# Kernel tuning notes

Measured on AMD Instinct MI355X. Metric: run time of the kernel, lower is better.

The kernel has to match this reference:

```python
import jax, jax.numpy as jnp
import numpy as np

B, N, IN_DIM = 64, 4096, 128
D = 128          # slot_size
S = 7            # num_slots
ITERS = 3
HID = 256        # mlp_hdim
EPS = 1e-8       # renorm epsilon
LN_EPS = 1e-5    # torch LayerNorm default


def _ln(x, g, b):
    m = jnp.mean(x, axis=-1, keepdims=True)
    v = jnp.mean((x - m) ** 2, axis=-1, keepdims=True)
    return (x - m) * jax.lax.rsqrt(v + LN_EPS) * g + b


def setup_inputs() -> dict:
    key = jax.random.key(0)
    ks = jax.random.split(key, 16)
    s = 0.02
    return {
        "x": jax.random.normal(ks[0], (B, N, IN_DIM), jnp.float32),
        "noise": jax.random.normal(ks[1], (B, S, D), jnp.float32),
        "Wq": jax.random.normal(ks[2], (D, D), jnp.float32) * s,
        "Wk": jax.random.normal(ks[3], (D, IN_DIM), jnp.float32) * s,
        "Wv": jax.random.normal(ks[4], (D, IN_DIM), jnp.float32) * s,
        "ln_in_g": jnp.ones((IN_DIM,), jnp.float32),
        "ln_in_b": jnp.zeros((IN_DIM,), jnp.float32),
        "ln_slots_g": jnp.ones((D,), jnp.float32),
        "ln_slots_b": jnp.zeros((D,), jnp.float32),
        "ln_mlp_g": jnp.ones((D,), jnp.float32),
        "ln_mlp_b": jnp.zeros((D,), jnp.float32),
        "W_ih": jax.random.normal(ks[5], (3 * D, D), jnp.float32) * s,
        "W_hh": jax.random.normal(ks[6], (3 * D, D), jnp.float32) * s,
        "b_ih": jnp.zeros((3 * D,), jnp.float32),
        "b_hh": jnp.zeros((3 * D,), jnp.float32),
        "W1": jax.random.normal(ks[7], (HID, D), jnp.float32) * s,
        "b1": jnp.zeros((HID,), jnp.float32),
        "W2": jax.random.normal(ks[8], (D, HID), jnp.float32) * s,
        "b2": jnp.zeros((D,), jnp.float32),
        "mu": jax.random.normal(ks[9], (1, 1, D), jnp.float32) * s,
        "logsigma": jax.random.normal(ks[10], (1, D), jnp.float32) * s,
    }


def reference(x, noise, Wq, Wk, Wv, ln_in_g, ln_in_b, ln_slots_g, ln_slots_b,
              ln_mlp_g, ln_mlp_b, W_ih, W_hh, b_ih, b_hh, W1, b1, W2, b2,
              mu, logsigma):
    xn = _ln(x, ln_in_g, ln_in_b)              # (B,N,IN)
    k = xn @ Wk.T                              # (B,N,D)
    v = xn @ Wv.T                              # (B,N,D)

    scale = jax.nn.softplus(logsigma)[None] + 1e-5   # (1,1,D)
    slots = mu + scale * noise                 # rsample, (B,S,D)

    def gru(u, h):
        gx = u @ W_ih.T + b_ih                 # (B*S, 3D)
        gh = h @ W_hh.T + b_hh
        xr, xz, xn_ = jnp.split(gx, 3, axis=-1)
        hr, hz, hn = jnp.split(gh, 3, axis=-1)
        r = jax.nn.sigmoid(xr + hr)
        z = jax.nn.sigmoid(xz + hz)
        n = jnp.tanh(xn_ + r * hn)
        return (1.0 - z) * n + z * h

    inv_sqrt_d = D ** -0.5
    for _ in range(ITERS):
        slots_prev = slots
        sn = _ln(slots, ln_slots_g, ln_slots_b)
        q = sn @ Wq.T                          # (B,S,D)
        scores = inv_sqrt_d * jnp.einsum('bnd,bsd->bns', k, q)
        attn = jax.nn.softmax(scores, axis=-1)           # over slots
        attn = attn + EPS
        attn = attn / jnp.sum(attn, axis=1, keepdims=True)  # renorm over inputs
        updates = jnp.einsum('bns,bnd->bsd', attn, v)    # (B,S,D)
        h = gru(updates.reshape(-1, D), slots_prev.reshape(-1, D))
        slots = h.reshape(x.shape[0], S, D)
        slots = _ln(slots, ln_mlp_g, ln_mlp_b)
        slots = slots + (jax.nn.relu(slots @ W1.T + b1) @ W2.T + b2)
    return slots
```

## Files before the change

### kernel.cpp

```cpp
#include <hip/hip_runtime.h>
#include <hip/hip_bf16.h>
#include <stdint.h>

#define B_ 64
#define N_ 4096
#define D_ 128
#define S_ 7
#define EPS_ 1e-8f
#define LN_EPS_ 1e-5f

typedef float  f32x4  __attribute__((ext_vector_type(4)));
typedef __bf16 bf16x8 __attribute__((ext_vector_type(8)));

#define WIH_OFF 0
#define WHH_OFF 49152
#define W1_OFF  98304
#define W2_OFF  131072
#define WQ_OFF  163840
#define WBF_TOT 180224

__device__ __forceinline__ uint16_t f2bfbits(float f) {
    uint32_t x = __float_as_uint(f);
    return (uint16_t)((x + 0x7fffu + ((x >> 16) & 1u)) >> 16);
}
__device__ __forceinline__ uint32_t pk2(float a, float b) {
    return (uint32_t)f2bfbits(a) | ((uint32_t)f2bfbits(b) << 16);
}

__global__ __launch_bounds__(256) void k_prep(
    const float* __restrict__ noise, const float* __restrict__ Wk,
    const float* __restrict__ Wv, const float* __restrict__ mu,
    const float* __restrict__ logsigma, const float* __restrict__ Wq,
    const float* __restrict__ lsg, const float* __restrict__ lsb,
    const float* __restrict__ Wih, const float* __restrict__ Whh,
    const float* __restrict__ W1, const float* __restrict__ W2,
    uint16_t* __restrict__ Wsw, float* __restrict__ slots,
    uint16_t* __restrict__ qbf, uint16_t* __restrict__ wbf) {
    const int t = threadIdx.x;
    const int tid = blockIdx.x * 256 + t;
    __shared__ float sn[128];
    __shared__ float red[2];
    {
        int row = blockIdx.x;
        int b = row / 7, s = row - b * 7;
        bool act = t < 128;
        float v = 0.f;
        if (act) {
            float sc = log1pf(__expf(logsigma[t])) + 1e-5f;
            v = mu[t] + sc * noise[row * 128 + t];
            slots[row * 128 + t] = v;
        }
        float sv = act ? v : 0.f;
        #pragma unroll
        for (int m = 1; m < 64; m <<= 1) sv += __shfl_xor(sv, m);
        if (act && (t & 63) == 0) red[t >> 6] = sv;
        __syncthreads();
        float mean = (red[0] + red[1]) * (1.0f / 128.0f);
        __syncthreads();
        float dv = act ? (v - mean) : 0.f;
        float sq = dv * dv;
        #pragma unroll
        for (int m = 1; m < 64; m <<= 1) sq += __shfl_xor(sq, m);
        if (act && (t & 63) == 0) red[t >> 6] = sq;
        __syncthreads();
        float var = (red[0] + red[1]) * (1.0f / 128.0f);
        if (act) sn[t] = dv * rsqrtf(var + LN_EPS_) * lsg[t] + lsb[t];
        __syncthreads();
        if (act) {
            const float4* wr = (const float4*)(Wq + t * 128);
            float acc = 0.f;
            #pragma unroll 8
            for (int j = 0; j < 32; ++j) {
                float4 w = wr[j];
                float4 s4 = *(const float4*)(sn + 4 * j);
                acc += w.x * s4.x + w.y * s4.y + w.z * s4.z + w.w * s4.w;
            }
            qbf[(b * 16 + s) * 128 + t] = f2bfbits(acc * 0.08838834764831843f);
        }
    }
    if (tid < 32768) {
        int j = tid & 7, ch = tid >> 3;
        int lane = ch & 63, k0 = (ch >> 6) & 3, wt = (ch >> 8) & 7, h = ch >> 11;
        int row = wt * 16 + (lane & 15);
        int col = k0 * 32 + (lane >> 4) * 8 + j;
        float w = h ? Wv[row * 128 + col] : Wk[row * 128 + col];
        Wsw[tid] = f2bfbits(w);
    }
    if (tid < 73728) {
        int bb = tid / 1152, rem = tid - bb * 1152;
        int s = 7 + (rem >> 7), d = rem & 127;
        qbf[(bb * 16 + s) * 128 + d] = 0;
    }
    for (int e = tid; e < WBF_TOT; e += 448 * 256) {
        const float* W; int C, el;
        if (e < WHH_OFF)      { W = Wih; C = 128; el = e; }
        else if (e < W1_OFF)  { W = Whh; C = 128; el = e - WHH_OFF; }
        else if (e < W2_OFF)  { W = W1;  C = 128; el = e - W1_OFF; }
        else if (e < WQ_OFF)  { W = W2;  C = 256; el = e - W2_OFF; }
        else                  { W = Wq;  C = 128; el = e - WQ_OFF; }
        int tile = el >> 9, within = el & 511;
        int lp = within >> 3, j = within & 7;
        int lm = lp & 15, qd = lp >> 4;
        int ktN = C >> 5;
        int ot = tile / ktN, kt = tile - ot * ktN;
        wbf[e] = f2bfbits(W[(ot * 16 + lm) * C + kt * 32 + qd * 8 + j]);
    }
}

__global__ __launch_bounds__(256) void k_proj(
    const float* __restrict__ x, const uint16_t* __restrict__ Wsw,
    const float* __restrict__ lng, const float* __restrict__ lnb,
    uint16_t* __restrict__ kfrag, uint16_t* __restrict__ vfrag) {
    __shared__ __align__(16) uint16_t wlds[16384];
    const int t = threadIdx.x, wv = t >> 6, lane = t & 63;
    const int lm = lane & 15, qd = lane >> 4;
    const long row0 = (long)blockIdx.x * 64;
    const int b = (int)(row0 >> 12);
    const int nloc = (int)(row0 & 4095);

    uint4 wst[8];
    #pragma unroll
    for (int i = 0; i < 8; ++i)
        wst[i] = *(const uint4*)(Wsw + (i * 256 + t) * 8);

    const long xrow = row0 + wv * 16 + lm;
    const float* xp = x + xrow * 128 + qd * 8;
    f32x4 xa[8];
    #pragma unroll
    for (int k0 = 0; k0 < 4; ++k0) {
        xa[2 * k0]     = *(const f32x4*)(xp + k0 * 32);
        xa[2 * k0 + 1] = *(const f32x4*)(xp + k0 * 32 + 4);
    }
    #pragma unroll
    for (int i = 0; i < 8; ++i)
        *(uint4*)(wlds + (i * 256 + t) * 8) = wst[i];
    #pragma unroll
    for (int i = 0; i < 8; ++i)
        wst[i] = *(const uint4*)(Wsw + 16384 + (i * 256 + t) * 8);

    float s = 0.f, sq = 0.f;
    #pragma unroll
    for (int i = 0; i < 8; ++i)
        #pragma unroll
        for (int c = 0; c < 4; ++c) { float v = xa[i][c]; s += v; sq += v * v; }
    s  += __shfl_xor(s, 16);  s  += __shfl_xor(s, 32);
    sq += __shfl_xor(sq, 16); sq += __shfl_xor(sq, 32);
    float mean = s * (1.0f / 128.0f);
    float var  = sq * (1.0f / 128.0f) - mean * mean;
    float rs   = rsqrtf(var + LN_EPS_);

    bf16x8 xf[4];
    #pragma unroll
    for (int k0 = 0; k0 < 4; ++k0) {
        const float* gp = lng + k0 * 32 + qd * 8;
        const float* bp = lnb + k0 * 32 + qd * 8;
        f32x4 g0 = *(const f32x4*)(gp), g1 = *(const f32x4*)(gp + 4);
        f32x4 b0 = *(const f32x4*)(bp), b1 = *(const f32x4*)(bp + 4);
        #pragma unroll
        for (int c = 0; c < 4; ++c) {
            xf[k0][c]     = (__bf16)((xa[2 * k0][c]     - mean) * rs * g0[c] + b0[c]);
            xf[k0][4 + c] = (__bf16)((xa[2 * k0 + 1][c] - mean) * rs * g1[c] + b1[c]);
        }
    }
    __syncthreads();

    const int ntg = (int)(row0 >> 4) + wv;
    #pragma unroll
    for (int mt = 0; mt < 8; ++mt) {
        f32x4 acc = {0.f, 0.f, 0.f, 0.f};
        #pragma unroll
        for (int k0 = 0; k0 < 4; ++k0) {
            bf16x8 wf = *(const bf16x8*)(wlds + ((mt * 4 + k0) * 64 + lane) * 8);
            acc = __builtin_amdgcn_mfma_f32_16x16x32_bf16(wf, xf[k0], acc, 0, 0, 0);
        }
        uint2 st; st.x = pk2(acc[0], acc[1]); st.y = pk2(acc[2], acc[3]);
        long base = ((long)(ntg * 4 + (mt >> 1))) * 512
                  + (lm + 16 * ((2 * mt + (qd >> 1)) & 3)) * 8 + (qd & 1) * 4;
        *(uint2*)(kfrag + base) = st;
    }
    __syncthreads();

    #pragma unroll
    for (int i = 0; i < 8; ++i)
        *(uint4*)(wlds + (i * 256 + t) * 8) = wst[i];
    __syncthreads();

    #pragma unroll
    for (int nt = 0; nt < 8; ++nt) {
        f32x4 acc = {0.f, 0.f, 0.f, 0.f};
        #pragma unroll
        for (int k0 = 0; k0 < 4; ++k0) {
            bf16x8 wf = *(const bf16x8*)(wlds + ((nt * 4 + k0) * 64 + lane) * 8);
            acc = __builtin_amdgcn_mfma_f32_16x16x32_bf16(xf[k0], wf, acc, 0, 0, 0);
        }
        uint2 st; st.x = pk2(acc[0], acc[1]); st.y = pk2(acc[2], acc[3]);
        long tile = (long)(b * 8 + nt) * 128 + (nloc >> 5) + (wv >> 1);
        long base = tile * 512
                  + (lm + 16 * (((wv & 1) * 2 + (qd >> 1)) & 3)) * 8 + (qd & 1) * 4;
        *(uint2*)(vfrag + base) = st;
    }
}

__global__ __launch_bounds__(512) void k_attn(
    const uint16_t* __restrict__ kfrag, const uint16_t* __restrict__ vfrag,
    const uint16_t* __restrict__ qbf,
    float* __restrict__ upart, float* __restrict__ cpart) {
    __shared__ __align__(16) uint16_t als[8][1024];
    __shared__ __align__(16) float part[8][7][132];
    __shared__ float bsum[8][8];
    const int t = threadIdx.x, wv = t >> 6, lane = t & 63;
    const int lm = lane & 15, qd = lane >> 4;
    const int b = blockIdx.x >> 3, chunk = blockIdx.x & 7;
    const int rb = chunk * 512 + wv * 64;
    const long gn = (long)b * N_ + rb;

    bf16x8 bq[4];
    #pragma unroll
    for (int k0 = 0; k0 < 4; ++k0)
        bq[k0] = *(const bf16x8*)(qbf + b * 2048 + lm * 128 + k0 * 32 + qd * 8);

    float csl = 0.f;
    #pragma unroll
    for (int mt = 0; mt < 4; ++mt) {
        f32x4 acc = {0.f, 0.f, 0.f, 0.f};
        long tb = ((gn >> 4) + mt) * 4;
        #pragma unroll
        for (int k0 = 0; k0 < 4; ++k0) {
            bf16x8 a = *(const bf16x8*)(kfrag + (tb + k0) * 512 + lane * 8);
            acc = __builtin_amdgcn_mfma_f32_16x16x32_bf16(a, bq[k0], acc, 0, 0, 0);
        }
        uint16_t pb[4];
        #pragma unroll
        for (int r = 0; r < 4; ++r) {
            float sc = acc[r];
            float scm = (lm < 7) ? sc : -1e30f;
            #pragma unroll
            for (int m = 1; m < 16; m <<= 1) scm = fmaxf(scm, __shfl_xor(scm, m));
            float e = (lm < 7) ? __expf(sc - scm) : 0.f;
            float tot = e;
            #pragma unroll
            for (int m = 1; m < 16; m <<= 1) tot += __shfl_xor(tot, m);
            float a_ = e / tot + EPS_;
            if (lm < 7) csl += a_;
            pb[r] = f2bfbits(a_);
        }
        int elem = (mt >> 1) * 512 + (((mt & 1) * 2 + (qd >> 1)) * 16 + lm) * 8 + (qd & 1) * 4;
        uint2 pw; pw.x = (uint32_t)pb[0] | ((uint32_t)pb[1] << 16);
        pw.y = (uint32_t)pb[2] | ((uint32_t)pb[3] << 16);
        *(uint2*)(&als[wv][elem]) = pw;
    }
    csl += __shfl_xor(csl, 16); csl += __shfl_xor(csl, 32);
    if (lane < 7) bsum[wv][lane] = csl;
    __syncthreads();

    bf16x8 afr0 = *(const bf16x8*)(&als[wv][lane * 8]);
    bf16x8 afr1 = *(const bf16x8*)(&als[wv][512 + lane * 8]);
    f32x4 uacc[8];
    #pragma unroll
    for (int i = 0; i < 8; ++i) uacc[i] = (f32x4){0.f, 0.f, 0.f, 0.f};
    #pragma unroll
    for (int nt = 0; nt < 8; ++nt) {
        long tb = ((long)(b * 8 + nt) * 128 + (rb >> 5)) * 512;
        bf16x8 v0 = *(const bf16x8*)(vfrag + tb + lane * 8);
        bf16x8 v1 = *(const bf16x8*)(vfrag + tb + 512 + lane * 8);
        uacc[nt] = __builtin_amdgcn_mfma_f32_16x16x32_bf16(v0, afr0, uacc[nt], 0, 0, 0);
        uacc[nt] = __builtin_amdgcn_mfma_f32_16x16x32_bf16(v1, afr1, uacc[nt], 0, 0, 0);
    }
    if (lm < 7) {
        #pragma unroll
        for (int nt = 0; nt < 8; ++nt)
            *(f32x4*)&part[wv][lm][nt * 16 + qd * 4] = uacc[nt];
    }
    __syncthreads();
    if (t < 128) {
        #pragma unroll
        for (int s = 0; s < 7; ++s) {
            float v = 0.f;
            #pragma unroll
            for (int w = 0; w < 8; ++w) v += part[w][s][t];
            upart[((b * 8 + chunk) * 7 + s) * 128 + t] = v;
        }
    }
    if (t < 7) {
        float c = 0.f;
        #pragma unroll
        for (int w = 0; w < 8; ++w) c += bsum[w][t];
        cpart[(b * 8 + chunk) * 7 + t] = c;
    }
}

__global__ __launch_bounds__(256) void k_fused(
    const float* __restrict__ upart, const float* __restrict__ cpart,
    float* __restrict__ slots, const uint16_t* __restrict__ wbf,
    const float* __restrict__ bih, const float* __restrict__ bhh,
    const float* __restrict__ gm, const float* __restrict__ bm,
    const float* __restrict__ b1, const float* __restrict__ b2,
    const float* __restrict__ lsg, const float* __restrict__ lsb,
    uint16_t* __restrict__ qbf, float* __restrict__ dst, int hasq) {
    __shared__ float uf[16][132];
    __shared__ float hf[16][132];
    __shared__ float slf[16][132];
    __shared__ float hidl[16][264];
    __shared__ float glg[7][776];
    __shared__ float csl[7];
    const int b = blockIdx.x;
    const int t = threadIdx.x, wv = t >> 6, lane = t & 63;
    const int lm = lane & 15, qd = lane >> 4;

    if (t < 7) {
        float c = 0.f;
        #pragma unroll
        for (int i = 0; i < 8; ++i) c += cpart[(b * 8 + i) * 7 + t];
        csl[t] = c;
    }
    __syncthreads();
    for (int idx = t; idx < 896; idx += 256) {
        int s = idx >> 7, d = idx & 127;
        float acc = 0.f;
        #pragma unroll
        for (int i = 0; i < 8; ++i) acc += upart[((b * 8 + i) * 7 + s) * 128 + d];
        uf[s][d] = acc / csl[s];
        hf[s][d] = slots[(b * 7 + s) * 128 + d];
    }
    __syncthreads();

    bf16x8 au[4], ah[4];
    #pragma unroll
    for (int k0 = 0; k0 < 4; ++k0)
        #pragma unroll
        for (int j = 0; j < 8; ++j) {
            au[k0][j] = (__bf16)uf[lm][k0 * 32 + qd * 8 + j];
            ah[k0][j] = (__bf16)hf[lm][k0 * 32 + qd * 8 + j];
        }

    {
        const int ih = (wv < 2);
        const uint16_t* W = wbf + (ih ? WIH_OFF : WHH_OFF);
        const int base = ih ? 0 : 384;
        const int w2 = wv & 1;
        #pragma unroll
        for (int i = 0; i < 12; ++i) {
            int ot = w2 * 12 + i;
            f32x4 acc = {0.f, 0.f, 0.f, 0.f};
            #pragma unroll
            for (int k0 = 0; k0 < 4; ++k0) {
                bf16x8 bf = *(const bf16x8*)(W + ((ot * 4 + k0) << 9) + lane * 8);
                acc = __builtin_amdgcn_mfma_f32_16x16x32_bf16(ih ? au[k0] : ah[k0], bf, acc, 0, 0, 0);
            }
            #pragma unroll
            for (int r = 0; r < 4; ++r) {
                int s = qd * 4 + r;
                if (s < 7) glg[s][base + ot * 16 + lm] = acc[r];
            }
        }
    }
    __syncthreads();

    for (int idx = t; idx < 896; idx += 256) {
        int s = idx >> 7, d = idx & 127;
        float xr = glg[s][d] + bih[d];
        float xz = glg[s][128 + d] + bih[128 + d];
        float xn = glg[s][256 + d] + bih[256 + d];
        float hr = glg[s][384 + d] + bhh[d];
        float hz = glg[s][512 + d] + bhh[128 + d];
        float hnn = glg[s][640 + d] + bhh[256 + d];
        float r = 1.f / (1.f + __expf(-(xr + hr)));
        float z = 1.f / (1.f + __expf(-(xz + hz)));
        float n = tanhf(xn + r * hnn);
        uf[s][d] = (1.f - z) * n + z * hf[s][d];
    }
    __syncthreads();

    for (int s = wv; s < 7; s += 4) {
        float a0 = uf[s][2 * lane], a1 = uf[s][2 * lane + 1];
        float sm = a0 + a1, sq = a0 * a0 + a1 * a1;
        #pragma unroll
        for (int m = 1; m < 64; m <<= 1) { sm += __shfl_xor(sm, m); sq += __shfl_xor(sq, m); }
        float mean = sm * (1.0f / 128.0f);
        float var = sq * (1.0f / 128.0f) - mean * mean;
        float rs = rsqrtf(var + LN_EPS_);
        slf[s][2 * lane]     = (a0 - mean) * rs * gm[2 * lane] + bm[2 * lane];
        slf[s][2 * lane + 1] = (a1 - mean) * rs * gm[2 * lane + 1] + bm[2 * lane + 1];
    }
    __syncthreads();

    bf16x8 as_[4];
    #pragma unroll
    for (int k0 = 0; k0 < 4; ++k0)
        #pragma unroll
        for (int j = 0; j < 8; ++j) as_[k0][j] = (__bf16)slf[lm][k0 * 32 + qd * 8 + j];
    #pragma unroll
    for (int i = 0; i < 4; ++i) {
        int ot = wv * 4 + i;
        f32x4 acc = {0.f, 0.f, 0.f, 0.f};
        #pragma unroll
        for (int k0 = 0; k0 < 4; ++k0) {
            bf16x8 bf = *(const bf16x8*)(wbf + W1_OFF + ((ot * 4 + k0) << 9) + lane * 8);
            acc = __builtin_amdgcn_mfma_f32_16x16x32_bf16(as_[k0], bf, acc, 0, 0, 0);
        }
        #pragma unroll
        for (int r = 0; r < 4; ++r) {
            int s = qd * 4 + r;
            if (s < 7) hidl[s][ot * 16 + lm] = fmaxf(acc[r] + b1[ot * 16 + lm], 0.f);
        }
    }
    __syncthreads();

    bf16x8 ahd[8];
    #pragma unroll
    for (int k0 = 0; k0 < 8; ++k0)
        #pragma unroll
        for (int j = 0; j < 8; ++j) ahd[k0][j] = (__bf16)hidl[lm][k0 * 32 + qd * 8 + j];
    #pragma unroll
    for (int i = 0; i < 2; ++i) {
        int ot = wv * 2 + i;
        f32x4 acc = {0.f, 0.f, 0.f, 0.f};
        #pragma unroll
        for (int k0 = 0; k0 < 8; ++k0) {
            bf16x8 bf = *(const bf16x8*)(wbf + W2_OFF + ((ot * 8 + k0) << 9) + lane * 8);
            acc = __builtin_amdgcn_mfma_f32_16x16x32_bf16(ahd[k0], bf, acc, 0, 0, 0);
        }
        #pragma unroll
        for (int r = 0; r < 4; ++r) {
            int s = qd * 4 + r;
            if (s < 7) {
                float v = slf[s][ot * 16 + lm] + acc[r] + b2[ot * 16 + lm];
                hf[s][ot * 16 + lm] = v;
                dst[(b * 7 + s) * 128 + ot * 16 + lm] = v;
            }
        }
    }
    if (hasq) {
        __syncthreads();
        for (int s = wv; s < 7; s += 4) {
            float a0 = hf[s][2 * lane], a1 = hf[s][2 * lane + 1];
            float sm = a0 + a1, sq = a0 * a0 + a1 * a1;
            #pragma unroll
            for (int m = 1; m < 64; m <<= 1) { sm += __shfl_xor(sm, m); sq += __shfl_xor(sq, m); }
            float mean = sm * (1.0f / 128.0f);
            float var = sq * (1.0f / 128.0f) - mean * mean;
            float rs = rsqrtf(var + LN_EPS_);
            uf[s][2 * lane]     = (a0 - mean) * rs * lsg[2 * lane] + lsb[2 * lane];
            uf[s][2 * lane + 1] = (a1 - mean) * rs * lsg[2 * lane + 1] + lsb[2 * lane + 1];
        }
        __syncthreads();
        bf16x8 an[4];
        #pragma unroll
        for (int k0 = 0; k0 < 4; ++k0)
            #pragma unroll
            for (int j = 0; j < 8; ++j) an[k0][j] = (__bf16)uf[lm][k0 * 32 + qd * 8 + j];
        #pragma unroll
        for (int i = 0; i < 2; ++i) {
            int ot = wv * 2 + i;
            f32x4 acc = {0.f, 0.f, 0.f, 0.f};
            #pragma unroll
            for (int k0 = 0; k0 < 4; ++k0) {
                bf16x8 bf = *(const bf16x8*)(wbf + WQ_OFF + ((ot * 4 + k0) << 9) + lane * 8);
                acc = __builtin_amdgcn_mfma_f32_16x16x32_bf16(an[k0], bf, acc, 0, 0, 0);
            }
            #pragma unroll
            for (int r = 0; r < 4; ++r) {
                int s = qd * 4 + r;
                if (s < 7)
                    qbf[(b * 16 + s) * 128 + ot * 16 + lm] = f2bfbits(acc[r] * 0.08838834764831843f);
            }
        }
    }
}

extern "C" void kernel_launch(void* const* d_in, const int* in_sizes, int n_in,
                              void* d_out, int out_size, void* d_ws, size_t ws_size,
                              hipStream_t stream) {
    const float* x    = (const float*)d_in[0];
    const float* nz   = (const float*)d_in[1];
    const float* Wq   = (const float*)d_in[2];
    const float* Wk   = (const float*)d_in[3];
    const float* Wv   = (const float*)d_in[4];
    const float* ling = (const float*)d_in[5];
    const float* linb = (const float*)d_in[6];
    const float* lsg  = (const float*)d_in[7];
    const float* lsb  = (const float*)d_in[8];
    const float* lmg  = (const float*)d_in[9];
    const float* lmb  = (const float*)d_in[10];
    const float* Wih  = (const float*)d_in[11];
    const float* Whh  = (const float*)d_in[12];
    const float* bih  = (const float*)d_in[13];
    const float* bhh  = (const float*)d_in[14];
    const float* W1   = (const float*)d_in[15];
    const float* b1   = (const float*)d_in[16];
    const float* W2   = (const float*)d_in[17];
    const float* b2   = (const float*)d_in[18];
    const float* mu   = (const float*)d_in[19];
    const float* lsig = (const float*)d_in[20];

    char* wsb = (char*)d_ws;
    uint16_t* kfrag = (uint16_t*)(wsb);
    uint16_t* vfrag = (uint16_t*)(wsb + (size_t)67108864);
    uint16_t* Wsw   = (uint16_t*)(wsb + (size_t)134217728);
    uint16_t* qbf   = (uint16_t*)(wsb + (size_t)134283264);
    float*    slots = (float*)  (wsb + (size_t)134545408);
    float*    upart = (float*)  (wsb + (size_t)134774784);
    float*    cpart = (float*)  (wsb + (size_t)136609792);
    uint16_t* wbf   = (uint16_t*)(wsb + (size_t)136624128);

    k_prep<<<448, 256, 0, stream>>>(nz, Wk, Wv, mu, lsig, Wq, lsg, lsb,
                                    Wih, Whh, W1, W2, Wsw, slots, qbf, wbf);
    k_proj<<<4096, 256, 0, stream>>>(x, Wsw, ling, linb, kfrag, vfrag);
    for (int it = 0; it < 3; ++it) {
        float* dst = (it == 2) ? (float*)d_out : slots;
        k_attn<<<512, 512, 0, stream>>>(kfrag, vfrag, qbf, upart, cpart);
        k_fused<<<64, 256, 0, stream>>>(upart, cpart, slots, wbf, bih, bhh,
                                        lmg, lmb, b1, b2, lsg, lsb,
                                        qbf, dst, (it < 2) ? 1 : 0);
    }
}
```

Baseline: 414.3 us.

## Fold Wk into query and Wv into update; attend directly over normalized inputs

```diff
diff --git a/kernel.cpp b/kernel.cpp
--- a/kernel.cpp
+++ b/kernel.cpp
@@ -8,6 +8,7 @@
 #define S_ 7
 #define EPS_ 1e-8f
 #define LN_EPS_ 1e-5f
+#define SC_INV 0.08838834764831843f
 
 typedef float  f32x4  __attribute__((ext_vector_type(4)));
 typedef __bf16 bf16x8 __attribute__((ext_vector_type(8)));
@@ -17,7 +18,9 @@
 #define W1_OFF  98304
 #define W2_OFF  131072
 #define WQ_OFF  163840
-#define WBF_TOT 180224
+#define WKT_OFF 180224
+#define WV_OFF  196608
+#define WBF_TOT 212992
 
 __device__ __forceinline__ uint16_t f2bfbits(float f) {
     uint32_t x = __float_as_uint(f);
@@ -27,266 +30,226 @@
     return (uint32_t)f2bfbits(a) | ((uint32_t)f2bfbits(b) << 16);
 }
 
-__global__ __launch_bounds__(256) void k_prep(
+__global__ __launch_bounds__(256) void k_init(
     const float* __restrict__ noise, const float* __restrict__ Wk,
-    const float* __restrict__ Wv, const float* __restrict__ mu,
-    const float* __restrict__ logsigma, const float* __restrict__ Wq,
-    const float* __restrict__ lsg, const float* __restrict__ lsb,
+    const float* __restrict__ mu, const float* __restrict__ logsigma,
+    const float* __restrict__ Wq, const float* __restrict__ lsg,
+    const float* __restrict__ lsb,
     const float* __restrict__ Wih, const float* __restrict__ Whh,
     const float* __restrict__ W1, const float* __restrict__ W2,
-    uint16_t* __restrict__ Wsw, float* __restrict__ slots,
-    uint16_t* __restrict__ qbf, uint16_t* __restrict__ wbf) {
+    const float* __restrict__ Wv,
+    float* __restrict__ slots, uint16_t* __restrict__ kqbf,
+    uint16_t* __restrict__ wbf) {
     const int t = threadIdx.x;
     const int tid = blockIdx.x * 256 + t;
-    __shared__ float sn[128];
+    const int row = blockIdx.x;
+    const int b = row / 7, s = row - b * 7;
+    __shared__ float sn[128], qr[128];
     __shared__ float red[2];
-    {
-        int row = blockIdx.x;
-        int b = row / 7, s = row - b * 7;
-        bool act = t < 128;
-        float v = 0.f;
-        if (act) {
-            float sc = log1pf(__expf(logsigma[t])) + 1e-5f;
-            v = mu[t] + sc * noise[row * 128 + t];
-            slots[row * 128 + t] = v;
-        }
-        float sv = act ? v : 0.f;
-        #pragma unroll
-        for (int m = 1; m < 64; m <<= 1) sv += __shfl_xor(sv, m);
-        if (act && (t & 63) == 0) red[t >> 6] = sv;
-        __syncthreads();
-        float mean = (red[0] + red[1]) * (1.0f / 128.0f);
-        __syncthreads();
-        float dv = act ? (v - mean) : 0.f;
-        float sq = dv * dv;
-        #pragma unroll
-        for (int m = 1; m < 64; m <<= 1) sq += __shfl_xor(sq, m);
-        if (act && (t & 63) == 0) red[t >> 6] = sq;
-        __syncthreads();
-        float var = (red[0] + red[1]) * (1.0f / 128.0f);
-        if (act) sn[t] = dv * rsqrtf(var + LN_EPS_) * lsg[t] + lsb[t];
-        __syncthreads();
-        if (act) {
-            const float4* wr = (const float4*)(Wq + t * 128);
-            float acc = 0.f;
-            #pragma unroll 8
-            for (int j = 0; j < 32; ++j) {
-                float4 w = wr[j];
-                float4 s4 = *(const float4*)(sn + 4 * j);
-                acc += w.x * s4.x + w.y * s4.y + w.z * s4.z + w.w * s4.w;
-            }
-            qbf[(b * 16 + s) * 128 + t] = f2bfbits(acc * 0.08838834764831843f);
-        }
-    }
-    if (tid < 32768) {
-        int j = tid & 7, ch = tid >> 3;
-        int lane = ch & 63, k0 = (ch >> 6) & 3, wt = (ch >> 8) & 7, h = ch >> 11;
-        int row = wt * 16 + (lane & 15);
-        int col = k0 * 32 + (lane >> 4) * 8 + j;
-        float w = h ? Wv[row * 128 + col] : Wk[row * 128 + col];
-        Wsw[tid] = f2bfbits(w);
+    bool act = t < 128;
+    float v = 0.f;
+    if (act) {
+        float sc = log1pf(__expf(logsigma[t])) + 1e-5f;
+        v = mu[t] + sc * noise[row * 128 + t];
+        slots[row * 128 + t] = v;
+    }
+    float sv = act ? v : 0.f;
+    #pragma unroll
+    for (int m = 1; m < 64; m <<= 1) sv += __shfl_xor(sv, m);
+    if (act && (t & 63) == 0) red[t >> 6] = sv;
+    __syncthreads();
+    float mean = (red[0] + red[1]) * (1.0f / 128.0f);
+    __syncthreads();
+    float dv = act ? (v - mean) : 0.f;
+    float sq = dv * dv;
+    #pragma unroll
+    for (int m = 1; m < 64; m <<= 1) sq += __shfl_xor(sq, m);
+    if (act && (t & 63) == 0) red[t >> 6] = sq;
+    __syncthreads();
+    float var = (red[0] + red[1]) * (1.0f / 128.0f);
+    if (act) sn[t] = dv * rsqrtf(var + LN_EPS_) * lsg[t] + lsb[t];
+    __syncthreads();
+    if (act) {
+        const float4* wr = (const float4*)(Wq + t * 128);
+        float acc = 0.f;
+        #pragma unroll 8
+        for (int j = 0; j < 32; ++j) {
+            float4 w = wr[j];
+            float4 s4 = *(const float4*)(sn + 4 * j);
+            acc += w.x * s4.x + w.y * s4.y + w.z * s4.z + w.w * s4.w;
+        }
+        qr[t] = acc;
+    }
+    __syncthreads();
+    if (act) {
+        float kq = 0.f;
+        #pragma unroll 8
+        for (int o = 0; o < 128; ++o) kq += qr[o] * Wk[o * 128 + t];
+        int elem = (t >> 5) * 512 + (s + 16 * ((t >> 3) & 3)) * 8 + (t & 7);
+        kqbf[b * 2048 + elem] = f2bfbits(kq * SC_INV);
     }
     if (tid < 73728) {
         int bb = tid / 1152, rem = tid - bb * 1152;
-        int s = 7 + (rem >> 7), d = rem & 127;
-        qbf[(bb * 16 + s) * 128 + d] = 0;
+        int sp = 7 + (rem >> 7), d = rem & 127;
+        int elem = (d >> 5) * 512 + (sp + 16 * ((d >> 3) & 3)) * 8 + (d & 7);
+        kqbf[bb * 2048 + elem] = 0;
     }
     for (int e = tid; e < WBF_TOT; e += 448 * 256) {
-        const float* W; int C, el;
+        const float* W; int C, el, mode = 0;
         if (e < WHH_OFF)      { W = Wih; C = 128; el = e; }
         else if (e < W1_OFF)  { W = Whh; C = 128; el = e - WHH_OFF; }
         else if (e < W2_OFF)  { W = W1;  C = 128; el = e - W1_OFF; }
         else if (e < WQ_OFF)  { W = W2;  C = 256; el = e - W2_OFF; }
-        else                  { W = Wq;  C = 128; el = e - WQ_OFF; }
+        else if (e < WKT_OFF) { W = Wq;  C = 128; el = e - WQ_OFF; }
+        else if (e < WV_OFF)  { W = Wk;  C = 128; el = e - WKT_OFF; mode = 1; }
+        else                  { W = Wv;  C = 128; el = e - WV_OFF; }
         int tile = el >> 9, within = el & 511;
         int lp = within >> 3, j = within & 7;
-        int lm = lp & 15, qd = lp >> 4;
-        int ktN = C >> 5;
-        int ot = tile / ktN, kt = tile - ot * ktN;
-        wbf[e] = f2bfbits(W[(ot * 16 + lm) * C + kt * 32 + qd * 8 + j]);
-    }
-}
-
-__global__ __launch_bounds__(256) void k_proj(
-    const float* __restrict__ x, const uint16_t* __restrict__ Wsw,
-    const float* __restrict__ lng, const float* __restrict__ lnb,
-    uint16_t* __restrict__ kfrag, uint16_t* __restrict__ vfrag) {
-    __shared__ __align__(16) uint16_t wlds[16384];
+        int lm_ = lp & 15, qd_ = lp >> 4;
+        float w;
+        if (!mode) {
+            int ktN = C >> 5, ot = tile / ktN, kt = tile - ot * ktN;
+            w = W[(ot * 16 + lm_) * C + kt * 32 + qd_ * 8 + j];
+        } else {
+            int dt = tile >> 2, kt = tile & 3;
+            w = W[(kt * 32 + qd_ * 8 + j) * 128 + dt * 16 + lm_];
+        }
+        wbf[e] = f2bfbits(w);
+    }
+}
+
+__global__ __launch_bounds__(256) void k_prep_xn(
+    const float* __restrict__ x, const float* __restrict__ lng,
+    const float* __restrict__ lnb, uint16_t* __restrict__ xn) {
     const int t = threadIdx.x, wv = t >> 6, lane = t & 63;
     const int lm = lane & 15, qd = lane >> 4;
-    const long row0 = (long)blockIdx.x * 64;
-    const int b = (int)(row0 >> 12);
-    const int nloc = (int)(row0 & 4095);
-
-    uint4 wst[8];
-    #pragma unroll
-    for (int i = 0; i < 8; ++i)
-        wst[i] = *(const uint4*)(Wsw + (i * 256 + t) * 8);
-
-    const long xrow = row0 + wv * 16 + lm;
-    const float* xp = x + xrow * 128 + qd * 8;
+    const long row = (long)blockIdx.x * 64 + wv * 16 + lm;
+    const long ntile = (long)blockIdx.x * 4 + wv;
+    const float* xp = x + row * 128 + qd * 4;
     f32x4 xa[8];
     #pragma unroll
-    for (int k0 = 0; k0 < 4; ++k0) {
-        xa[2 * k0]     = *(const f32x4*)(xp + k0 * 32);
-        xa[2 * k0 + 1] = *(const f32x4*)(xp + k0 * 32 + 4);
-    }
-    #pragma unroll
-    for (int i = 0; i < 8; ++i)
-        *(uint4*)(wlds + (i * 256 + t) * 8) = wst[i];
-    #pragma unroll
-    for (int i = 0; i < 8; ++i)
-        wst[i] = *(const uint4*)(Wsw + 16384 + (i * 256 + t) * 8);
-
+    for (int c = 0; c < 8; ++c) xa[c] = *(const f32x4*)(xp + c * 16);
     float s = 0.f, sq = 0.f;
     #pragma unroll
-    for (int i = 0; i < 8; ++i)
-        #pragma unroll
-        for (int c = 0; c < 4; ++c) { float v = xa[i][c]; s += v; sq += v * v; }
+    for (int c = 0; c < 8; ++c)
+        #pragma unroll
+        for (int r = 0; r < 4; ++r) { float v = xa[c][r]; s += v; sq += v * v; }
     s  += __shfl_xor(s, 16);  s  += __shfl_xor(s, 32);
     sq += __shfl_xor(sq, 16); sq += __shfl_xor(sq, 32);
     float mean = s * (1.0f / 128.0f);
     float var  = sq * (1.0f / 128.0f) - mean * mean;
     float rs   = rsqrtf(var + LN_EPS_);
-
-    bf16x8 xf[4];
-    #pragma unroll
-    for (int k0 = 0; k0 < 4; ++k0) {
-        const float* gp = lng + k0 * 32 + qd * 8;
-        const float* bp = lnb + k0 * 32 + qd * 8;
-        f32x4 g0 = *(const f32x4*)(gp), g1 = *(const f32x4*)(gp + 4);
-        f32x4 b0 = *(const f32x4*)(bp), b1 = *(const f32x4*)(bp + 4);
-        #pragma unroll
-        for (int c = 0; c < 4; ++c) {
-            xf[k0][c]     = (__bf16)((xa[2 * k0][c]     - mean) * rs * g0[c] + b0[c]);
-            xf[k0][4 + c] = (__bf16)((xa[2 * k0 + 1][c] - mean) * rs * g1[c] + b1[c]);
-        }
-    }
-    __syncthreads();
-
-    const int ntg = (int)(row0 >> 4) + wv;
-    #pragma unroll
-    for (int mt = 0; mt < 8; ++mt) {
-        f32x4 acc = {0.f, 0.f, 0.f, 0.f};
-        #pragma unroll
-        for (int k0 = 0; k0 < 4; ++k0) {
-            bf16x8 wf = *(const bf16x8*)(wlds + ((mt * 4 + k0) * 64 + lane) * 8);
-            acc = __builtin_amdgcn_mfma_f32_16x16x32_bf16(wf, xf[k0], acc, 0, 0, 0);
-        }
-        uint2 st; st.x = pk2(acc[0], acc[1]); st.y = pk2(acc[2], acc[3]);
-        long base = ((long)(ntg * 4 + (mt >> 1))) * 512
-                  + (lm + 16 * ((2 * mt + (qd >> 1)) & 3)) * 8 + (qd & 1) * 4;
-        *(uint2*)(kfrag + base) = st;
-    }
-    __syncthreads();
-
-    #pragma unroll
-    for (int i = 0; i < 8; ++i)
-        *(uint4*)(wlds + (i * 256 + t) * 8) = wst[i];
-    __syncthreads();
-
-    #pragma unroll
-    for (int nt = 0; nt < 8; ++nt) {
-        f32x4 acc = {0.f, 0.f, 0.f, 0.f};
-        #pragma unroll
-        for (int k0 = 0; k0 < 4; ++k0) {
-            bf16x8 wf = *(const bf16x8*)(wlds + ((nt * 4 + k0) * 64 + lane) * 8);
-            acc = __builtin_amdgcn_mfma_f32_16x16x32_bf16(xf[k0], wf, acc, 0, 0, 0);
-        }
-        uint2 st; st.x = pk2(acc[0], acc[1]); st.y = pk2(acc[2], acc[3]);
-        long tile = (long)(b * 8 + nt) * 128 + (nloc >> 5) + (wv >> 1);
-        long base = tile * 512
-                  + (lm + 16 * (((wv & 1) * 2 + (qd >> 1)) & 3)) * 8 + (qd & 1) * 4;
-        *(uint2*)(vfrag + base) = st;
-    }
-}
-
-__global__ __launch_bounds__(512) void k_attn(
-    const uint16_t* __restrict__ kfrag, const uint16_t* __restrict__ vfrag,
-    const uint16_t* __restrict__ qbf,
+    #pragma unroll
+    for (int c = 0; c < 8; ++c) {
+        f32x4 g  = *(const f32x4*)(lng + c * 16 + qd * 4);
+        f32x4 bb = *(const f32x4*)(lnb + c * 16 + qd * 4);
+        float v0 = (xa[c][0] - mean) * rs * g[0] + bb[0];
+        float v1 = (xa[c][1] - mean) * rs * g[1] + bb[1];
+        float v2 = (xa[c][2] - mean) * rs * g[2] + bb[2];
+        float v3 = (xa[c][3] - mean) * rs * g[3] + bb[3];
+        uint2 st; st.x = pk2(v0, v1); st.y = pk2(v2, v3);
+        long elem = (ntile * 4 + (c >> 1)) * 512
+                  + (lm + 16 * (2 * (c & 1) + (qd >> 1))) * 8 + 4 * (qd & 1);
+        *(uint2*)(xn + elem) = st;
+    }
+}
+
+__global__ __launch_bounds__(256) void k_attn(
+    const uint16_t* __restrict__ xn, const uint16_t* __restrict__ kqbf,
     float* __restrict__ upart, float* __restrict__ cpart) {
-    __shared__ __align__(16) uint16_t als[8][1024];
-    __shared__ __align__(16) float part[8][7][132];
-    __shared__ float bsum[8][8];
+    __shared__ __align__(16) uint16_t xns[4][32 * 132];
+    __shared__ __align__(16) uint16_t als[4][512];
+    __shared__ float part[4][7][132];
+    __shared__ float bsum[4][8];
     const int t = threadIdx.x, wv = t >> 6, lane = t & 63;
     const int lm = lane & 15, qd = lane >> 4;
-    const int b = blockIdx.x >> 3, chunk = blockIdx.x & 7;
-    const int rb = chunk * 512 + wv * 64;
-    const long gn = (long)b * N_ + rb;
-
-    bf16x8 bq[4];
+    const int b = blockIdx.x >> 4, chunk = blockIdx.x & 15;
+    const int ntb = b * 256 + chunk * 16 + wv * 4;
+
+    bf16x8 kqf[4];
     #pragma unroll
     for (int k0 = 0; k0 < 4; ++k0)
-        bq[k0] = *(const bf16x8*)(qbf + b * 2048 + lm * 128 + k0 * 32 + qd * 8);
-
+        kqf[k0] = *(const bf16x8*)(kqbf + b * 2048 + k0 * 512 + lane * 8);
+
+    uint16_t* xw = xns[wv];
+    f32x4 uacc[8];
+    #pragma unroll
+    for (int i = 0; i < 8; ++i) uacc[i] = (f32x4){0.f, 0.f, 0.f, 0.f};
     float csl = 0.f;
-    #pragma unroll
-    for (int mt = 0; mt < 4; ++mt) {
-        f32x4 acc = {0.f, 0.f, 0.f, 0.f};
-        long tb = ((gn >> 4) + mt) * 4;
-        #pragma unroll
-        for (int k0 = 0; k0 < 4; ++k0) {
-            bf16x8 a = *(const bf16x8*)(kfrag + (tb + k0) * 512 + lane * 8);
-            acc = __builtin_amdgcn_mfma_f32_16x16x32_bf16(a, bq[k0], acc, 0, 0, 0);
-        }
-        uint16_t pb[4];
-        #pragma unroll
-        for (int r = 0; r < 4; ++r) {
-            float sc = acc[r];
-            float scm = (lm < 7) ? sc : -1e30f;
-            #pragma unroll
-            for (int m = 1; m < 16; m <<= 1) scm = fmaxf(scm, __shfl_xor(scm, m));
-            float e = (lm < 7) ? __expf(sc - scm) : 0.f;
-            float tot = e;
-            #pragma unroll
-            for (int m = 1; m < 16; m <<= 1) tot += __shfl_xor(tot, m);
-            float a_ = e / tot + EPS_;
-            if (lm < 7) csl += a_;
-            pb[r] = f2bfbits(a_);
-        }
-        int elem = (mt >> 1) * 512 + (((mt & 1) * 2 + (qd >> 1)) * 16 + lm) * 8 + (qd & 1) * 4;
-        uint2 pw; pw.x = (uint32_t)pb[0] | ((uint32_t)pb[1] << 16);
-        pw.y = (uint32_t)pb[2] | ((uint32_t)pb[3] << 16);
-        *(uint2*)(&als[wv][elem]) = pw;
+
+    #pragma unroll
+    for (int sub = 0; sub < 2; ++sub) {
+        bf16x8 xf[2][4];
+        #pragma unroll
+        for (int nt = 0; nt < 2; ++nt)
+            #pragma unroll
+            for (int k0 = 0; k0 < 4; ++k0)
+                xf[nt][k0] = *(const bf16x8*)(xn +
+                    ((long)(ntb + sub * 2 + nt) * 4 + k0) * 512 + lane * 8);
+        #pragma unroll
+        for (int nt = 0; nt < 2; ++nt)
+            #pragma unroll
+            for (int k0 = 0; k0 < 4; ++k0) {
+                int base = (nt * 16 + lm) * 132 + k0 * 32 + qd * 8;
+                const uint2* src = (const uint2*)&xf[nt][k0];
+                *(uint2*)(xw + base)     = src[0];
+                *(uint2*)(xw + base + 4) = src[1];
+            }
+        #pragma unroll
+        for (int mt = 0; mt < 2; ++mt) {
+            f32x4 acc = {0.f, 0.f, 0.f, 0.f};
+            #pragma unroll
+            for (int k0 = 0; k0 < 4; ++k0)
+                acc = __builtin_amdgcn_mfma_f32_16x16x32_bf16(xf[mt][k0], kqf[k0], acc, 0, 0, 0);
+            uint16_t pb[4];
+            #pragma unroll
+            for (int r = 0; r < 4; ++r) {
+                float sc = acc[r];
+                float scm = (lm < 7) ? sc : -1e30f;
+                #pragma unroll
+                for (int m = 1; m < 16; m <<= 1) scm = fmaxf(scm, __shfl_xor(scm, m));
+                float e = (lm < 7) ? __expf(sc - scm) : 0.f;
+                float tot = e;
+                #pragma unroll
+                for (int m = 1; m < 16; m <<= 1) tot += __shfl_xor(tot, m);
+                float a_ = e / tot + EPS_;
+                if (lm < 7) csl += a_;
+                pb[r] = f2bfbits(a_);
+            }
+            int elem = (lm + 16 * (2 * mt + (qd >> 1))) * 8 + 4 * (qd & 1);
+            uint2 pw; pw.x = (uint32_t)pb[0] | ((uint32_t)pb[1] << 16);
+            pw.y = (uint32_t)pb[2] | ((uint32_t)pb[3] << 16);
+            *(uint2*)(&als[wv][elem]) = pw;
+        }
+        bf16x8 afr = *(const bf16x8*)(&als[wv][lane * 8]);
+        #pragma unroll
+        for (int dt = 0; dt < 8; ++dt) {
+            bf16x8 bfr;
+            #pragma unroll
+            for (int j = 0; j < 8; ++j)
+                bfr[j] = ((const __bf16*)xw)[(qd * 8 + j) * 132 + dt * 16 + lm];
+            uacc[dt] = __builtin_amdgcn_mfma_f32_16x16x32_bf16(afr, bfr, uacc[dt], 0, 0, 0);
+        }
     }
     csl += __shfl_xor(csl, 16); csl += __shfl_xor(csl, 32);
     if (lane < 7) bsum[wv][lane] = csl;
-    __syncthreads();
-
-    bf16x8 afr0 = *(const bf16x8*)(&als[wv][lane * 8]);
-    bf16x8 afr1 = *(const bf16x8*)(&als[wv][512 + lane * 8]);
-    f32x4 uacc[8];
-    #pragma unroll
-    for (int i = 0; i < 8; ++i) uacc[i] = (f32x4){0.f, 0.f, 0.f, 0.f};
-    #pragma unroll
-    for (int nt = 0; nt < 8; ++nt) {
-        long tb = ((long)(b * 8 + nt) * 128 + (rb >> 5)) * 512;
-        bf16x8 v0 = *(const bf16x8*)(vfrag + tb + lane * 8);
-        bf16x8 v1 = *(const bf16x8*)(vfrag + tb + 512 + lane * 8);
-        uacc[nt] = __builtin_amdgcn_mfma_f32_16x16x32_bf16(v0, afr0, uacc[nt], 0, 0, 0);
-        uacc[nt] = __builtin_amdgcn_mfma_f32_16x16x32_bf16(v1, afr1, uacc[nt], 0, 0, 0);
-    }
-    if (lm < 7) {
-        #pragma unroll
-        for (int nt = 0; nt < 8; ++nt)
-            *(f32x4*)&part[wv][lm][nt * 16 + qd * 4] = uacc[nt];
-    }
+    #pragma unroll
+    for (int dt = 0; dt < 8; ++dt)
+        #pragma unroll
+        for (int r = 0; r < 4; ++r) {
+            int s = qd * 4 + r;
+            if (s < 7) part[wv][s][dt * 16 + lm] = uacc[dt][r];
+        }
     __syncthreads();
     if (t < 128) {
         #pragma unroll
         for (int s = 0; s < 7; ++s) {
-            float v = 0.f;
-            #pragma unroll
-            for (int w = 0; w < 8; ++w) v += part[w][s][t];
-            upart[((b * 8 + chunk) * 7 + s) * 128 + t] = v;
-        }
-    }
-    if (t < 7) {
-        float c = 0.f;
-        #pragma unroll
-        for (int w = 0; w < 8; ++w) c += bsum[w][t];
-        cpart[(b * 8 + chunk) * 7 + t] = c;
-    }
+            float v = part[0][s][t] + part[1][s][t] + part[2][s][t] + part[3][s][t];
+            upart[((b * 16 + chunk) * 7 + s) * 128 + t] = v;
+        }
+    }
+    if (t < 7)
+        cpart[(b * 16 + chunk) * 7 + t] = bsum[0][t] + bsum[1][t] + bsum[2][t] + bsum[3][t];
 }
 
 __global__ __launch_bounds__(256) void k_fused(
@@ -296,7 +259,7 @@
     const float* __restrict__ gm, const float* __restrict__ bm,
     const float* __restrict__ b1, const float* __restrict__ b2,
     const float* __restrict__ lsg, const float* __restrict__ lsb,
-    uint16_t* __restrict__ qbf, float* __restrict__ dst, int hasq) {
+    uint16_t* __restrict__ kqbf, float* __restrict__ dst, int hasq) {
     __shared__ float uf[16][132];
     __shared__ float hf[16][132];
     __shared__ float slf[16][132];
@@ -310,17 +273,40 @@
     if (t < 7) {
         float c = 0.f;
         #pragma unroll
-        for (int i = 0; i < 8; ++i) c += cpart[(b * 8 + i) * 7 + t];
+        for (int i = 0; i < 16; ++i) c += cpart[(b * 16 + i) * 7 + t];
         csl[t] = c;
     }
-    __syncthreads();
     for (int idx = t; idx < 896; idx += 256) {
         int s = idx >> 7, d = idx & 127;
         float acc = 0.f;
         #pragma unroll
-        for (int i = 0; i < 8; ++i) acc += upart[((b * 8 + i) * 7 + s) * 128 + d];
-        uf[s][d] = acc / csl[s];
+        for (int i = 0; i < 16; ++i) acc += upart[((b * 16 + i) * 7 + s) * 128 + d];
+        slf[s][d] = acc;
         hf[s][d] = slots[(b * 7 + s) * 128 + d];
+    }
+    __syncthreads();
+
+    {
+        bf16x8 apb[4];
+        #pragma unroll
+        for (int k0 = 0; k0 < 4; ++k0)
+            #pragma unroll
+            for (int j = 0; j < 8; ++j) apb[k0][j] = (__bf16)slf[lm][k0 * 32 + qd * 8 + j];
+        #pragma unroll
+        for (int i = 0; i < 2; ++i) {
+            int dt = wv * 2 + i;
+            f32x4 acc = {0.f, 0.f, 0.f, 0.f};
+            #pragma unroll
+            for (int k0 = 0; k0 < 4; ++k0) {
+                bf16x8 bf = *(const bf16x8*)(wbf + WV_OFF + ((dt * 4 + k0) << 9) + lane * 8);
+                acc = __builtin_amdgcn_mfma_f32_16x16x32_bf16(apb[k0], bf, acc, 0, 0, 0);
+            }
+            #pragma unroll
+            for (int r = 0; r < 4; ++r) {
+                int s = qd * 4 + r;
+                if (s < 7) uf[s][dt * 16 + lm] = acc[r] / csl[s];
+            }
+        }
     }
     __syncthreads();
 
@@ -332,7 +318,6 @@
             au[k0][j] = (__bf16)uf[lm][k0 * 32 + qd * 8 + j];
             ah[k0][j] = (__bf16)hf[lm][k0 * 32 + qd * 8 + j];
         }
-
     {
         const int ih = (wv < 2);
         const uint16_t* W = wbf + (ih ? WIH_OFF : WHH_OFF);
@@ -360,13 +345,13 @@
         int s = idx >> 7, d = idx & 127;
         float xr = glg[s][d] + bih[d];
         float xz = glg[s][128 + d] + bih[128 + d];
-        float xn = glg[s][256 + d] + bih[256 + d];
+        float xg = glg[s][256 + d] + bih[256 + d];
         float hr = glg[s][384 + d] + bhh[d];
         float hz = glg[s][512 + d] + bhh[128 + d];
-        float hnn = glg[s][640 + d] + bhh[256 + d];
+        float hg = glg[s][640 + d] + bhh[256 + d];
         float r = 1.f / (1.f + __expf(-(xr + hr)));
         float z = 1.f / (1.f + __expf(-(xz + hz)));
-        float n = tanhf(xn + r * hnn);
+        float n = tanhf(xg + r * hg);
         uf[s][d] = (1.f - z) * n + z * hf[s][d];
     }
     __syncthreads();
@@ -461,9 +446,44 @@
             #pragma unroll
             for (int r = 0; r < 4; ++r) {
                 int s = qd * 4 + r;
-                if (s < 7)
-                    qbf[(b * 16 + s) * 128 + ot * 16 + lm] = f2bfbits(acc[r] * 0.08838834764831843f);
-            }
+                if (s < 7) slf[s][ot * 16 + lm] = acc[r];
+            }
+        }
+        __syncthreads();
+        bf16x8 aq[4];
+        #pragma unroll
+        for (int k0 = 0; k0 < 4; ++k0)
+            #pragma unroll
+            for (int j = 0; j < 8; ++j) aq[k0][j] = (__bf16)slf[lm][k0 * 32 + qd * 8 + j];
+        #pragma unroll
+        for (int i = 0; i < 2; ++i) {
+            int dt = wv * 2 + i;
+            f32x4 acc = {0.f, 0.f, 0.f, 0.f};
+            #pragma unroll
+            for (int k0 = 0; k0 < 4; ++k0) {
+                bf16x8 bf = *(const bf16x8*)(wbf + WKT_OFF + ((dt * 4 + k0) << 9) + lane * 8);
+                acc = __builtin_amdgcn_mfma_f32_16x16x32_bf16(aq[k0], bf, acc, 0, 0, 0);
+            }
+            #pragma unroll
+            for (int r = 0; r < 4; ++r) {
+                int s = qd * 4 + r;
+                if (s < 7) hidl[s][dt * 16 + lm] = acc[r];
+            }
+        }
+        __syncthreads();
+        {
+            int kt = t >> 6, lp = t & 63;
+            int lmp = lp & 15, qdp = lp >> 4;
+            uint16_t h[8];
+            #pragma unroll
+            for (int j = 0; j < 8; ++j)
+                h[j] = (lmp < 7) ? f2bfbits(hidl[lmp][kt * 32 + qdp * 8 + j] * SC_INV) : (uint16_t)0;
+            uint4 st;
+            st.x = (uint32_t)h[0] | ((uint32_t)h[1] << 16);
+            st.y = (uint32_t)h[2] | ((uint32_t)h[3] << 16);
+            st.z = (uint32_t)h[4] | ((uint32_t)h[5] << 16);
+            st.w = (uint32_t)h[6] | ((uint32_t)h[7] << 16);
+            *(uint4*)(kqbf + b * 2048 + t * 8) = st;
         }
     }
 }
@@ -494,23 +514,21 @@
     const float* lsig = (const float*)d_in[20];
 
     char* wsb = (char*)d_ws;
-    uint16_t* kfrag = (uint16_t*)(wsb);
-    uint16_t* vfrag = (uint16_t*)(wsb + (size_t)67108864);
-    uint16_t* Wsw   = (uint16_t*)(wsb + (size_t)134217728);
-    uint16_t* qbf   = (uint16_t*)(wsb + (size_t)134283264);
-    float*    slots = (float*)  (wsb + (size_t)134545408);
-    float*    upart = (float*)  (wsb + (size_t)134774784);
-    float*    cpart = (float*)  (wsb + (size_t)136609792);
-    uint16_t* wbf   = (uint16_t*)(wsb + (size_t)136624128);
-
-    k_prep<<<448, 256, 0, stream>>>(nz, Wk, Wv, mu, lsig, Wq, lsg, lsb,
-                                    Wih, Whh, W1, W2, Wsw, slots, qbf, wbf);
-    k_proj<<<4096, 256, 0, stream>>>(x, Wsw, ling, linb, kfrag, vfrag);
+    uint16_t* xn    = (uint16_t*)(wsb);
+    uint16_t* wbf   = (uint16_t*)(wsb + (size_t)67108864);
+    uint16_t* kqbf  = (uint16_t*)(wsb + (size_t)67534848);
+    float*    slots = (float*)  (wsb + (size_t)67796992);
+    float*    upart = (float*)  (wsb + (size_t)68026368);
+    float*    cpart = (float*)  (wsb + (size_t)71696384);
+
+    k_init<<<448, 256, 0, stream>>>(nz, Wk, mu, lsig, Wq, lsg, lsb,
+                                    Wih, Whh, W1, W2, Wv, slots, kqbf, wbf);
+    k_prep_xn<<<4096, 256, 0, stream>>>(x, ling, linb, xn);
     for (int it = 0; it < 3; ++it) {
         float* dst = (it == 2) ? (float*)d_out : slots;
-        k_attn<<<512, 512, 0, stream>>>(kfrag, vfrag, qbf, upart, cpart);
+        k_attn<<<1024, 256, 0, stream>>>(xn, kqbf, upart, cpart);
         k_fused<<<64, 256, 0, stream>>>(upart, cpart, slots, wbf, bih, bhh,
                                         lmg, lmb, b1, b2, lsg, lsb,
-                                        qbf, dst, (it < 2) ? 1 : 0);
-    }
-}
+                                        kqbf, dst, (it < 2) ? 1 : 0);
+    }
+}
```

New measurement: 376.1 us. 1.1x faster.
